# Performance work log

Hardware: AMD Instinct MI355X
Metric: run time of the kernel (lower is better)

Reference implementation:

```python
import jax, jax.numpy as jnp
import numpy as np

NP_, NG_ = 20000, 5000            # protein / go_annotation node counts
D_FEAT, D_HID, N_CLS = 512, 128, 1000
E_PP, E_PG, E_GP = 240000, 100000, 100000
NEG_SLOPE = -0.2                  # note: the repo default slope is negative
EPS = 1e-12


def _l2norm(x):
    n = jnp.linalg.norm(x, axis=1, keepdims=True)
    return x / jnp.maximum(n, EPS)


def _edge_softmax(logits, dst, n):
    # per-destination-node softmax over incoming edges, per feature channel
    m = jax.ops.segment_max(logits, dst, num_segments=n)
    e = jnp.exp(logits - m[dst])
    s = jax.ops.segment_sum(e, dst, num_segments=n)
    return e / s[dst]


def _type_attn(h_src, h_dst, src, dst, Wl, bl, Wr, br):
    # GCN-normalized aggregation onto dst nodes, then type-level attention logits,
    # broadcast back to edges (copy_u on the reversed relation graph).
    ns, nd = h_src.shape[0], h_dst.shape[0]
    ones = jnp.ones(src.shape[0], dtype=h_src.dtype)
    outdeg = jnp.clip(jax.ops.segment_sum(ones, src, num_segments=ns), 1.0)
    feat = h_src * (outdeg ** -0.5)[:, None]
    rst = jax.ops.segment_sum(feat[src], dst, num_segments=nd)
    indeg = jnp.clip(jax.ops.segment_sum(ones, dst, num_segments=nd), 1.0)
    rst = rst * (indeg ** -0.5)[:, None]
    ea = jax.nn.elu((h_dst @ Wl + bl) + (rst @ Wr + br))  # [nd, D_HID]
    return ea[dst]                                        # [E, D_HID]


def setup_inputs() -> dict:
    key = jax.random.key(0)
    ks = iter(jax.random.split(key, 40))

    def nrm(shape, s=0.05):
        return jax.random.normal(next(ks), shape, dtype=jnp.float32) * s

    def ri(n, hi):
        return jax.random.randint(next(ks), (n,), 0, hi, dtype=jnp.int32)

    zeros = lambda n: jnp.zeros((n,), jnp.float32)
    return dict(
        x_protein=jax.random.normal(next(ks), (NP_, D_FEAT), dtype=jnp.float32),
        x_go=jax.random.normal(next(ks), (NG_, N_CLS), dtype=jnp.float32),
        src_pp=ri(E_PP, NP_), dst_pp=ri(E_PP, NP_),
        src_pg=ri(E_PG, NP_), dst_pg=ri(E_PG, NG_),
        src_gp=ri(E_GP, NG_), dst_gp=ri(E_GP, NP_),
        W1p=nrm((D_FEAT, D_HID)), b1p=zeros(D_HID),
        W1g=nrm((N_CLS, D_HID)), b1g=zeros(D_HID),
        Wl_p=nrm((D_HID, D_HID)), bl_p=zeros(D_HID),
        Wl_g=nrm((D_HID, D_HID)), bl_g=zeros(D_HID),
        Wr_p=nrm((D_HID, D_HID)), br_p=zeros(D_HID),
        Wr_g=nrm((D_HID, D_HID)), br_g=zeros(D_HID),
        Wnl=nrm((D_HID, D_HID)), bnl=zeros(D_HID),
        Wnr=nrm((D_HID, D_HID)), bnr=zeros(D_HID),
        Wfc=nrm((D_HID, N_CLS)), bfc=zeros(N_CLS),
    )


def reference(x_protein, x_go, src_pp, dst_pp, src_pg, dst_pg, src_gp, dst_gp,
              W1p, b1p, W1g, b1g, Wl_p, bl_p, Wl_g, bl_g,
              Wr_p, br_p, Wr_g, br_g, Wnl, bnl, Wnr, bnr, Wfc, bfc):
    # input projection + row-wise l2 norm (dropout disabled / eval mode)
    hp = _l2norm(x_protein @ W1p + b1p)   # [NP, D_HID]
    hg = _l2norm(x_go @ W1g + b1g)        # [NG, D_HID]

    # ---- TypeAttention over each canonical etype ----
    a_pp = _type_attn(hp, hp, src_pp, dst_pp, Wl_p, bl_p, Wr_p, br_p)
    a_pg = _type_attn(hp, hg, src_pg, dst_pg, Wl_g, bl_g, Wr_p, br_p)
    a_gp = _type_attn(hg, hp, src_gp, dst_gp, Wl_p, bl_p, Wr_g, br_g)

    # homogeneous view: proteins [0,NP), go_annotation [NP,NP+NG)
    gsrc = jnp.concatenate([src_pp, src_pg, src_gp + NP_])
    gdst = jnp.concatenate([dst_pp, dst_pg + NP_, dst_gp])
    alpha = jnp.concatenate([a_pp, a_pg, a_gp], axis=0)   # [E, D_HID]
    n = NP_ + NG_
    alpha = _edge_softmax(alpha, gdst, n)

    # ---- NodeAttention on the homogeneous graph ----
    x = jnp.concatenate([hp, hg], axis=0)                 # [N, D_HID]
    hl = (x @ Wnl + bnl)[gsrc]
    hr = (x @ Wnr + bnr)[gdst]
    e = (hl + hr) * alpha
    e = jnp.where(e > 0, e, NEG_SLOPE * e)                # LeakyReLU(slope=-0.2)
    a = _edge_softmax(e, gdst, n)
    h = jax.ops.segment_sum(x[gsrc] * a, gdst, num_segments=n)

    out = h @ Wfc + bfc   # [N, N_CLS]; rows [:NP]=protein, [NP:]=go_annotation
    return out
```

## Files before the change

### kernel.cpp

```cpp
#include <hip/hip_runtime.h>
#include <math.h>

#define NP 20000
#define NG 5000
#define NTOT 25000
#define DF 512
#define NCLS 1000
#define DH 128
#define EPP 240000
#define EPG 100000
#define EGP 100000
#define ETOT 440000
#define FS 16
#define HB 16

typedef __attribute__((ext_vector_type(8))) __bf16 bf16x8;
typedef __attribute__((ext_vector_type(4))) float f32x4;

__device__ __forceinline__ void gl2lds16(const void* g, void* l) {
    __builtin_amdgcn_global_load_lds(
        (const __attribute__((address_space(1))) unsigned int*)g,
        (__attribute__((address_space(3))) unsigned int*)l, 16, 0, 0);
}

__device__ __forceinline__ float b2f(unsigned short u) {
    union { unsigned int i; float f; } c; c.i = ((unsigned int)u) << 16; return c.f;
}

__global__ __launch_bounds__(1024) void hist_part_kernel(
    const int* __restrict__ src_pp, const int* __restrict__ dst_pp,
    const int* __restrict__ src_pg, const int* __restrict__ dst_pg,
    const int* __restrict__ src_gp, const int* __restrict__ dst_gp,
    int* __restrict__ partial)
{
    __shared__ int bins[20000];
    const int job = blockIdx.y, b = blockIdx.x;
    const int* idx; int nbins, nedge; size_t pbase;
    switch (job) {
    case 0: idx = src_pp; nbins = 20000; nedge = EPP; pbase = 0;       break;
    case 1: idx = dst_pp; nbins = 20000; nedge = EPP; pbase = 320000;  break;
    case 2: idx = src_pg; nbins = 20000; nedge = EPG; pbase = 640000;  break;
    case 3: idx = dst_pg; nbins = 5000;  nedge = EPG; pbase = 960000;  break;
    case 4: idx = src_gp; nbins = 5000;  nedge = EGP; pbase = 1040000; break;
    default: idx = dst_gp; nbins = 20000; nedge = EGP; pbase = 1120000; break;
    }
    for (int i = threadIdx.x; i < nbins; i += 1024) bins[i] = 0;
    __syncthreads();
    const int chunk = (nedge + HB - 1) / HB;
    const int e0 = b * chunk, e1 = min(e0 + chunk, nedge);
    for (int e = e0 + threadIdx.x; e < e1; e += 1024) atomicAdd(&bins[idx[e]], 1);
    __syncthreads();
    int* dst = partial + pbase + (size_t)b * nbins;
    for (int i = threadIdx.x; i < nbins; i += 1024) dst[i] = bins[i];
}

__global__ __launch_bounds__(256) void hist_merge_kernel(const int* __restrict__ partial,
    int* __restrict__ outdeg_pp, int* __restrict__ indeg_pp,
    int* __restrict__ outdeg_pg, int* __restrict__ indeg_pg,
    int* __restrict__ outdeg_gp, int* __restrict__ indeg_gp,
    int* __restrict__ fill)
{
    const int job = blockIdx.y;
    const int bin = blockIdx.x * 256 + threadIdx.x;
    if (job == 6) {
        if (bin < NTOT * FS) fill[bin] = 0;
        return;
    }
    const int nbins = (job == 3 || job == 4) ? 5000 : 20000;
    if (bin >= nbins) return;
    size_t pbase; int* outp;
    switch (job) {
    case 0: pbase = 0;       outp = outdeg_pp; break;
    case 1: pbase = 320000;  outp = indeg_pp;  break;
    case 2: pbase = 640000;  outp = outdeg_pg; break;
    case 3: pbase = 960000;  outp = indeg_pg;  break;
    case 4: pbase = 1040000; outp = outdeg_gp; break;
    default: pbase = 1120000; outp = indeg_gp; break;
    }
    const int* p = partial + pbase + bin;
    int s = 0;
#pragma unroll
    for (int b = 0; b < HB; b++) s += p[(size_t)b * nbins];
    outp[bin] = s;
}

__global__ __launch_bounds__(1024) void scan_kernel(const int* __restrict__ indeg_pp,
                                                    const int* __restrict__ indeg_gp,
                                                    const int* __restrict__ indeg_pg,
                                                    int* __restrict__ row_ptr)
{
    __shared__ int part[1024];
    int t = threadIdx.x;
    const int CH = (NTOT + 1023) / 1024;
    int base = t * CH;
    auto cntf = [&](int idx) -> int {
        return (idx < NP) ? (indeg_pp[idx] + indeg_gp[idx]) : indeg_pg[idx - NP];
    };
    int s = 0;
    for (int i = 0; i < CH; i++) { int idx = base + i; if (idx < NTOT) s += cntf(idx); }
    part[t] = s;
    __syncthreads();
    for (int off = 1; off < 1024; off <<= 1) {
        int v = (t >= off) ? part[t - off] : 0;
        __syncthreads();
        part[t] += v;
        __syncthreads();
    }
    int run = (t == 0) ? 0 : part[t - 1];
    for (int i = 0; i < CH; i++) {
        int idx = base + i;
        if (idx < NTOT) { row_ptr[idx] = run; run += cntf(idx); }
    }
    if (t == 1023) row_ptr[NTOT] = part[1023];
}

__global__ void scatter_kernel(const int* __restrict__ src_pp, const int* __restrict__ dst_pp,
                               const int* __restrict__ src_pg, const int* __restrict__ dst_pg,
                               const int* __restrict__ src_gp, const int* __restrict__ dst_gp,
                               const int* __restrict__ outdeg_pp, const int* __restrict__ outdeg_pg,
                               const int* __restrict__ outdeg_gp,
                               const int* __restrict__ row_ptr, int* fill,
                               int2* __restrict__ edata)
{
    int e = blockIdx.x * blockDim.x + threadIdx.x;
    int s, d, t; float sc;
    if (e < EPP) {
        s = src_pp[e]; d = dst_pp[e]; t = 0;
        sc = rsqrtf((float)max(outdeg_pp[s], 1));
    } else if (e < EPP + EPG) {
        int i = e - EPP; s = src_pg[i]; d = NP + dst_pg[i]; t = 1;
        sc = rsqrtf((float)max(outdeg_pg[s], 1));
    } else if (e < ETOT) {
        int i = e - EPP - EPG; int sl = src_gp[i]; s = NP + sl; d = dst_gp[i]; t = 2;
        sc = rsqrtf((float)max(outdeg_gp[sl], 1));
    } else return;
    int pos = row_ptr[d] + atomicAdd(&fill[d * FS], 1);
    edata[pos] = make_int2(s | (t << 16), __float_as_int(sc));
}

__global__ __launch_bounds__(256) void conv_all_kernel(
    const float* __restrict__ xp, const float* __restrict__ xg,
    const float* W1p, const float* W1g, const float* Wlp, const float* Wrp, const float* Wrg,
    const float* Wnl, const float* Wnr, const float* Wfc,
    __bf16* __restrict__ xpb, __bf16* __restrict__ xgb,
    __bf16* w1pt, __bf16* w1gt, __bf16* wlpt, __bf16* wrpt, __bf16* wrgt,
    __bf16* wnlt, __bf16* wnrt, __bf16* wfct)
{
    const int b = blockIdx.x;
    if (b < 5008) {
        long long e = ((long long)b * 256 + threadIdx.x) * 8;
        int row = (int)(e >> 9), k = (int)(e & 511);
        __bf16 pk[8];
        if (row < NP) {
            f32x4 v0 = *(const f32x4*)(xp + (size_t)row * 512 + k);
            f32x4 v1 = *(const f32x4*)(xp + (size_t)row * 512 + k + 4);
#pragma unroll
            for (int i = 0; i < 4; i++) { pk[i] = (__bf16)v0[i]; pk[4 + i] = (__bf16)v1[i]; }
        } else {
#pragma unroll
            for (int i = 0; i < 8; i++) pk[i] = (__bf16)0.f;
        }
        *(bf16x8*)(xpb + e) = *(bf16x8*)pk;
        return;
    }
    if (b < 7536) {
        long long e = ((long long)(b - 5008) * 256 + threadIdx.x) * 8;
        int row = (int)(e >> 10), k = (int)(e & 1023);
        __bf16 pk[8];
        if (row < NG && k + 7 < 1000) {
            f32x4 v0 = *(const f32x4*)(xg + (size_t)row * 1000 + k);
            f32x4 v1 = *(const f32x4*)(xg + (size_t)row * 1000 + k + 4);
#pragma unroll
            for (int i = 0; i < 4; i++) { pk[i] = (__bf16)v0[i]; pk[4 + i] = (__bf16)v1[i]; }
        } else {
#pragma unroll
            for (int i = 0; i < 8; i++) {
                int kk = k + i;
                pk[i] = (__bf16)((row < NG && kk < 1000) ? xg[(size_t)row * 1000 + kk] : 0.f);
            }
        }
        *(bf16x8*)(xgb + e) = *(bf16x8*)pk;
        return;
    }
    int wb = b - 7536;
    int e;
    if (wb < 256)      { e = wb * 256 + threadIdx.x;          int n = e >> 9, k = e & 511;  w1pt[e] = (__bf16)W1p[(size_t)k * 128 + n]; }
    else if (wb < 768) { e = (wb - 256) * 256 + threadIdx.x;  int n = e >> 10, k = e & 1023; w1gt[e] = (__bf16)(k < 1000 ? W1g[(size_t)k * 128 + n] : 0.f); }
    else if (wb < 832) { e = (wb - 768) * 256 + threadIdx.x;  int n = e >> 7, k = e & 127;  wlpt[e] = (__bf16)Wlp[(size_t)k * 128 + n]; }
    else if (wb < 896) { e = (wb - 832) * 256 + threadIdx.x;  int n = e >> 7, k = e & 127;  wrpt[e] = (__bf16)Wrp[(size_t)k * 128 + n]; }
    else if (wb < 960) { e = (wb - 896) * 256 + threadIdx.x;  int n = e >> 7, k = e & 127;  wrgt[e] = (__bf16)Wrg[(size_t)k * 128 + n]; }
    else if (wb < 1024){ e = (wb - 960) * 256 + threadIdx.x;  int n = e >> 7, k = e & 127;  wnlt[e] = (__bf16)Wnl[(size_t)k * 128 + n]; }
    else if (wb < 1088){ e = (wb - 1024) * 256 + threadIdx.x; int n = e >> 7, k = e & 127;  wnrt[e] = (__bf16)Wnr[(size_t)k * 128 + n]; }
    else               { e = (wb - 1088) * 256 + threadIdx.x; int n = e >> 7, k = e & 127;  wfct[e] = (__bf16)(n < 1000 ? Wfc[(size_t)k * 1000 + n] : 0.f); }
}

struct GJob {
    const __bf16* A1;
    const __bf16* B1; const __bf16* B2;
    const float* b1; const float* b2;
    float* O1; __bf16* O2; __bf16* Ob;
    int M, N, Kp, ksteps;
};

template<int ACT, int DUALW, int EMIT>
__global__ __launch_bounds__(256) void gemm_bt(GJob j0, GJob j1, int split)
{
    __shared__ __align__(16) __bf16 As[64 * 32];
    __shared__ __align__(16) __bf16 Bs[128 * 32];
    __shared__ __align__(16) __bf16 B2s[DUALW ? 128 * 32 : 8];
    __shared__ float part[2][64];

    GJob j; int bx;
    if ((int)blockIdx.x < split) { j = j0; bx = blockIdx.x; }
    else { j = j1; bx = blockIdx.x - split; }

    const int tid = threadIdx.x;
    const int wave = tid >> 6, lane = tid & 63;
    const int wr = wave >> 1, wc = wave & 1;
    const int l15 = lane & 15, lh = lane >> 4;
    const int row0 = bx * 64;
    const int col0 = blockIdx.y * 128;

    const size_t aoff = (size_t)(row0 + (tid >> 2)) * j.Kp + (tid & 3) * 8;
    const size_t boff0 = (size_t)(col0 + (tid >> 2)) * j.Kp + (tid & 3) * 8;
    const size_t boff1 = boff0 + (size_t)64 * j.Kp;
    char* alds   = (char*)As + wave * 1024;
    char* blds0  = (char*)Bs + wave * 1024;
    char* blds1  = (char*)Bs + 4096 + wave * 1024;
    char* b2lds0 = (char*)B2s + wave * 1024;
    char* b2lds1 = (char*)B2s + 4096 + wave * 1024;

    f32x4 acc[2][4], acc2[2][4];
#pragma unroll
    for (int fm = 0; fm < 2; fm++)
#pragma unroll
        for (int fn = 0; fn < 4; fn++) {
            acc[fm][fn] = (f32x4)0.f;
            if (DUALW) acc2[fm][fn] = (f32x4)0.f;
        }

    for (int ks = 0; ks < j.ksteps; ks++) {
        const int k0 = ks * 32;
        __syncthreads();
        gl2lds16(j.A1 + aoff + k0, alds);
        gl2lds16(j.B1 + boff0 + k0, blds0);
        gl2lds16(j.B1 + boff1 + k0, blds1);
        if constexpr (DUALW) {
            gl2lds16(j.B2 + boff0 + k0, b2lds0);
            gl2lds16(j.B2 + boff1 + k0, b2lds1);
        }
        __syncthreads();

#pragma unroll
        for (int fm = 0; fm < 2; fm++) {
            bf16x8 a = *(const bf16x8*)&As[(wr * 32 + fm * 16 + l15) * 32 + lh * 8];
#pragma unroll
            for (int fn = 0; fn < 4; fn++) {
                bf16x8 b = *(const bf16x8*)&Bs[(wc * 64 + fn * 16 + l15) * 32 + lh * 8];
                acc[fm][fn] = __builtin_amdgcn_mfma_f32_16x16x32_bf16(a, b, acc[fm][fn], 0, 0, 0);
                if constexpr (DUALW) {
                    bf16x8 b2 = *(const bf16x8*)&B2s[(wc * 64 + fn * 16 + l15) * 32 + lh * 8];
                    acc2[fm][fn] = __builtin_amdgcn_mfma_f32_16x16x32_bf16(a, b2, acc2[fm][fn], 0, 0, 0);
                }
            }
        }
    }

    float bias[4], bias2[4];
#pragma unroll
    for (int fn = 0; fn < 4; fn++) {
        int col = col0 + wc * 64 + fn * 16 + l15;
        bias[fn] = 0.f; bias2[fn] = 0.f;
        if (col < j.N) {
            bias[fn] = j.b1[col];
            if (DUALW) bias2[fn] = j.b2[col];
        }
    }

    float vv[2][4][4];
#pragma unroll
    for (int fm = 0; fm < 2; fm++)
#pragma unroll
        for (int fn = 0; fn < 4; fn++)
#pragma unroll
            for (int r = 0; r < 4; r++) vv[fm][fn][r] = acc[fm][fn][r] + bias[fn];

    float scale[2][4];
#pragma unroll
    for (int fm = 0; fm < 2; fm++)
#pragma unroll
        for (int r = 0; r < 4; r++) scale[fm][r] = 1.f;

    if constexpr (ACT == 2) {
        float s[2][4];
#pragma unroll
        for (int fm = 0; fm < 2; fm++)
#pragma unroll
            for (int r = 0; r < 4; r++) {
                float v = 0.f;
#pragma unroll
                for (int fn = 0; fn < 4; fn++) v += vv[fm][fn][r] * vv[fm][fn][r];
                v += __shfl_xor(v, 1);
                v += __shfl_xor(v, 2);
                v += __shfl_xor(v, 4);
                v += __shfl_xor(v, 8);
                s[fm][r] = v;
            }
        __syncthreads();
        if (l15 == 0) {
#pragma unroll
            for (int fm = 0; fm < 2; fm++)
#pragma unroll
                for (int r = 0; r < 4; r++)
                    part[wc][wr * 32 + fm * 16 + lh * 4 + r] = s[fm][r];
        }
        __syncthreads();
#pragma unroll
        for (int fm = 0; fm < 2; fm++)
#pragma unroll
            for (int r = 0; r < 4; r++) {
                int rl = wr * 32 + fm * 16 + lh * 4 + r;
                float ss = part[0][rl] + part[1][rl];
                scale[fm][r] = 1.f / fmaxf(sqrtf(ss), 1e-12f);
            }
    }

#pragma unroll
    for (int fm = 0; fm < 2; fm++)
#pragma unroll
        for (int fn = 0; fn < 4; fn++)
#pragma unroll
            for (int r = 0; r < 4; r++) {
                int row = row0 + wr * 32 + fm * 16 + lh * 4 + r;
                int col = col0 + wc * 64 + fn * 16 + l15;
                if (row < j.M && col < j.N) {
                    float v = vv[fm][fn][r] * scale[fm][r];
                    if constexpr (EMIT == 0) j.O1[(size_t)row * j.N + col] = v;
                    if constexpr (EMIT == 2) j.Ob[(size_t)row * j.N + col] = (__bf16)v;
                    if constexpr (DUALW)
                        j.O2[(size_t)row * j.N + col] = (__bf16)(acc2[fm][fn][r] + bias2[fn]);
                }
            }
}

__global__ __launch_bounds__(256) void ea_wa_kernel(
    const __bf16* __restrict__ xb, const __bf16* __restrict__ rppb, const __bf16* __restrict__ rgpb,
    const __bf16* __restrict__ wl, const __bf16* __restrict__ wrp, const __bf16* __restrict__ wrg,
    const float* __restrict__ blp, const float* __restrict__ brp, const float* __restrict__ brg,
    const int* __restrict__ indeg_pp, const int* __restrict__ indeg_gp,
    float* __restrict__ wpp, float* __restrict__ wgp)
{
    __shared__ __align__(16) __bf16 A1s[64 * 32], A2s[64 * 32], A3s[64 * 32];
    __shared__ __align__(16) __bf16 B1s[128 * 32], B2s[128 * 32], B3s[128 * 32];

    const int tid = threadIdx.x;
    const int wave = tid >> 6, lane = tid & 63;
    const int wr = wave >> 1, wc = wave & 1;
    const int l15 = lane & 15, lh = lane >> 4;
    const int row0 = blockIdx.x * 64;

    const size_t aoff = (size_t)(row0 + (tid >> 2)) * 128 + (tid & 3) * 8;
    const size_t boff0 = (size_t)(tid >> 2) * 128 + (tid & 3) * 8;
    const size_t boff1 = boff0 + (size_t)64 * 128;
    char* a1 = (char*)A1s + wave * 1024;
    char* a2 = (char*)A2s + wave * 1024;
    char* a3 = (char*)A3s + wave * 1024;
    char* b1l0 = (char*)B1s + wave * 1024, *b1l1 = (char*)B1s + 4096 + wave * 1024;
    char* b2l0 = (char*)B2s + wave * 1024, *b2l1 = (char*)B2s + 4096 + wave * 1024;
    char* b3l0 = (char*)B3s + wave * 1024, *b3l1 = (char*)B3s + 4096 + wave * 1024;

    f32x4 accL[2][4], accP[2][4], accG[2][4];
#pragma unroll
    for (int fm = 0; fm < 2; fm++)
#pragma unroll
        for (int fn = 0; fn < 4; fn++) {
            accL[fm][fn] = (f32x4)0.f; accP[fm][fn] = (f32x4)0.f; accG[fm][fn] = (f32x4)0.f;
        }

    for (int ks = 0; ks < 4; ks++) {
        const int k0 = ks * 32;
        __syncthreads();
        gl2lds16(xb + aoff + k0, a1);
        gl2lds16(rppb + aoff + k0, a2);
        gl2lds16(rgpb + aoff + k0, a3);
        gl2lds16(wl + boff0 + k0, b1l0);  gl2lds16(wl + boff1 + k0, b1l1);
        gl2lds16(wrp + boff0 + k0, b2l0); gl2lds16(wrp + boff1 + k0, b2l1);
        gl2lds16(wrg + boff0 + k0, b3l0); gl2lds16(wrg + boff1 + k0, b3l1);
        __syncthreads();

#pragma unroll
        for (int fm = 0; fm < 2; fm++) {
            const int arow = (wr * 32 + fm * 16 + l15) * 32 + lh * 8;
            bf16x8 aL = *(const bf16x8*)&A1s[arow];
            bf16x8 aP = *(const bf16x8*)&A2s[arow];
            bf16x8 aG = *(const bf16x8*)&A3s[arow];
#pragma unroll
            for (int fn = 0; fn < 4; fn++) {
                const int brow = (wc * 64 + fn * 16 + l15) * 32 + lh * 8;
                bf16x8 bL = *(const bf16x8*)&B1s[brow];
                bf16x8 bP = *(const bf16x8*)&B2s[brow];
                bf16x8 bG = *(const bf16x8*)&B3s[brow];
                accL[fm][fn] = __builtin_amdgcn_mfma_f32_16x16x32_bf16(aL, bL, accL[fm][fn], 0, 0, 0);
                accP[fm][fn] = __builtin_amdgcn_mfma_f32_16x16x32_bf16(aP, bP, accP[fm][fn], 0, 0, 0);
                accG[fm][fn] = __builtin_amdgcn_mfma_f32_16x16x32_bf16(aG, bG, accG[fm][fn], 0, 0, 0);
            }
        }
    }

    float bp[4], bg[4];
#pragma unroll
    for (int fn = 0; fn < 4; fn++) {
        int col = wc * 64 + fn * 16 + l15;
        bp[fn] = blp[col] + brp[col];
        bg[fn] = blp[col] + brg[col];
    }

#pragma unroll
    for (int fm = 0; fm < 2; fm++)
#pragma unroll
        for (int r = 0; r < 4; r++) {
            int row = row0 + wr * 32 + fm * 16 + lh * 4 + r;
            int rr = min(row, NP - 1);
            int npp = indeg_pp[rr], ngp = indeg_gp[rr];
#pragma unroll
            for (int fn = 0; fn < 4; fn++) {
                int col = wc * 64 + fn * 16 + l15;
                float app = accL[fm][fn][r] + accP[fm][fn][r] + bp[fn];
                app = app > 0.f ? app : (__expf(app) - 1.f);
                float agp = accL[fm][fn][r] + accG[fm][fn][r] + bg[fn];
                agp = agp > 0.f ? agp : (__expf(agp) - 1.f);
                float wppv = 0.f, wgpv = 0.f;
                if (npp > 0 && ngp > 0) {
                    float mx = fmaxf(app, agp);
                    float ep = __expf(app - mx), eg = __expf(agp - mx);
                    float den = (float)npp * ep + (float)ngp * eg;
                    wppv = ep / den; wgpv = eg / den;
                } else if (npp > 0) wppv = 1.f / (float)npp;
                else if (ngp > 0) wgpv = 1.f / (float)ngp;
                if (row < NP) {
                    wpp[(size_t)row * DH + col] = wppv;
                    wgp[(size_t)row * DH + col] = wgpv;
                }
            }
        }
}

__global__ __launch_bounds__(128) void rst_agg_kernel(const __bf16* __restrict__ x,
                                                      const int* __restrict__ row_ptr,
                                                      const int2* __restrict__ edata,
                                                      const int* __restrict__ indeg_pp,
                                                      const int* __restrict__ indeg_gp,
                                                      __bf16* __restrict__ rppb, __bf16* __restrict__ rgpb)
{
    const int d = blockIdx.x;
    const int tid = threadIdx.x;
    const unsigned c2 = tid & 63;
    const int h = tid >> 6;
    const int beg = row_ptr[d], end = row_ptr[d + 1];
    const unsigned int* xu = (const unsigned int*)x;
    float spp0 = 0.f, spp1 = 0.f, sgp0 = 0.f, sgp1 = 0.f;

    int i = beg + h;
    for (; i + 6 < end; i += 8) {
        int2 e0 = edata[i], e1 = edata[i + 2], e2 = edata[i + 4], e3 = edata[i + 6];
        unsigned u0 = xu[(((unsigned)e0.x & 0xFFFFu) << 6) | c2];
        unsigned u1 = xu[(((unsigned)e1.x & 0xFFFFu) << 6) | c2];
        unsigned u2 = xu[(((unsigned)e2.x & 0xFFFFu) << 6) | c2];
        unsigned u3 = xu[(((unsigned)e3.x & 0xFFFFu) << 6) | c2];
#pragma unroll
        for (int k = 0; k < 4; k++) {
            unsigned u = (k == 0) ? u0 : (k == 1) ? u1 : (k == 2) ? u2 : u3;
            int2 e = (k == 0) ? e0 : (k == 1) ? e1 : (k == 2) ? e2 : e3;
            float lo = __uint_as_float(u << 16);
            float hi = __uint_as_float(u & 0xFFFF0000u);
            float sc = __int_as_float(e.y);
            if ((e.x >> 16) == 0) { spp0 = fmaf(lo, sc, spp0); spp1 = fmaf(hi, sc, spp1); }
            else                  { sgp0 = fmaf(lo, sc, sgp0); sgp1 = fmaf(hi, sc, sgp1); }
        }
    }
    for (; i < end; i += 2) {
        int2 e = edata[i];
        unsigned u = xu[(((unsigned)e.x & 0xFFFFu) << 6) | c2];
        float lo = __uint_as_float(u << 16);
        float hi = __uint_as_float(u & 0xFFFF0000u);
        float sc = __int_as_float(e.y);
        if ((e.x >> 16) == 0) { spp0 = fmaf(lo, sc, spp0); spp1 = fmaf(hi, sc, spp1); }
        else                  { sgp0 = fmaf(lo, sc, sgp0); sgp1 = fmaf(hi, sc, sgp1); }
    }

    __shared__ float red[4][64];
    if (h == 1) { red[0][c2] = spp0; red[1][c2] = spp1; red[2][c2] = sgp0; red[3][c2] = sgp1; }
    __syncthreads();
    if (h == 0) {
        spp0 += red[0][c2]; spp1 += red[1][c2]; sgp0 += red[2][c2]; sgp1 += red[3][c2];
        float ipp = rsqrtf((float)max(indeg_pp[d], 1));
        float igp = rsqrtf((float)max(indeg_gp[d], 1));
        union { unsigned u; __bf16 b[2]; } wp, wg;
        wp.b[0] = (__bf16)(spp0 * ipp); wp.b[1] = (__bf16)(spp1 * ipp);
        wg.b[0] = (__bf16)(sgp0 * igp); wg.b[1] = (__bf16)(sgp1 * igp);
        ((unsigned*)rppb)[((unsigned)d << 6) | c2] = wp.u;
        ((unsigned*)rgpb)[((unsigned)d << 6) | c2] = wg.u;
    }
}

__global__ __launch_bounds__(256) void pack_xhl_kernel(const unsigned int* __restrict__ xb2,
                                                       const unsigned int* __restrict__ hl2,
                                                       uint4* __restrict__ xhl4)
{
    int i = blockIdx.x * 256 + threadIdx.x;
    if (i >= 25024 * 128 / 4) return;
    unsigned int xa = xb2[i * 2], xbv = xb2[i * 2 + 1];
    unsigned int ha = hl2[i * 2], hbv = hl2[i * 2 + 1];
    uint4 o;
    o.x = (xa & 0xFFFFu) | (ha << 16);
    o.y = (xa >> 16) | (ha & 0xFFFF0000u);
    o.z = (xbv & 0xFFFFu) | (hbv << 16);
    o.w = (xbv >> 16) | (hbv & 0xFFFF0000u);
    xhl4[i] = o;
}

__global__ __launch_bounds__(128) void node_attn_kernel(const unsigned int* __restrict__ xhl,
                                                        const __bf16* __restrict__ hrb,
                                                        const float* __restrict__ wpp_arr,
                                                        const float* __restrict__ wgp_arr,
                                                        const int* __restrict__ indeg_pg,
                                                        const int* __restrict__ row_ptr,
                                                        const int2* __restrict__ edata,
                                                        __bf16* __restrict__ hb)
{
    const int d = blockIdx.x;
    const unsigned c = threadIdx.x;
    const int beg = row_ptr[d], end = row_ptr[d + 1];
    const float hrd = b2f(((const unsigned short*)hrb)[((size_t)d << 7) | c]);
    float wppv, wgpv;
    if (d < NP) {
        wppv = wpp_arr[((size_t)d << 7) | c];
        wgpv = wgp_arr[((size_t)d << 7) | c];
    } else {
        float w = 1.f / (float)max(indeg_pg[d - NP], 1);
        wppv = w; wgpv = w;
    }
    float ssum = 0.f, acc = 0.f;

    int i = beg;
    for (; i + 3 < end; i += 4) {
        int p0 = edata[i].x, p1 = edata[i + 1].x, p2 = edata[i + 2].x, p3 = edata[i + 3].x;
        unsigned int u0 = xhl[(((unsigned)p0 & 0xFFFFu) << 7) | c];
        unsigned int u1 = xhl[(((unsigned)p1 & 0xFFFFu) << 7) | c];
        unsigned int u2 = xhl[(((unsigned)p2 & 0xFFFFu) << 7) | c];
        unsigned int u3 = xhl[(((unsigned)p3 & 0xFFFFu) << 7) | c];
#pragma unroll
        for (int k = 0; k < 4; k++) {
            unsigned int u = (k == 0) ? u0 : (k == 1) ? u1 : (k == 2) ? u2 : u3;
            int p = (k == 0) ? p0 : (k == 1) ? p1 : (k == 2) ? p2 : p3;
            float xv  = __uint_as_float(u << 16);
            float hlv = __uint_as_float(u & 0xFFFF0000u);
            float al = ((p >> 16) == 0) ? wppv : wgpv;
            float e = (hlv + hrd) * al;
            e = fmaxf(e, -0.2f * e);
            float pw = __expf(e);
            ssum += pw;
            acc = fmaf(pw, xv, acc);
        }
    }
    for (; i < end; i++) {
        int p = edata[i].x;
        unsigned int u = xhl[(((unsigned)p & 0xFFFFu) << 7) | c];
        float xv  = __uint_as_float(u << 16);
        float hlv = __uint_as_float(u & 0xFFFF0000u);
        float al = ((p >> 16) == 0) ? wppv : wgpv;
        float e = (hlv + hrd) * al;
        e = fmaxf(e, -0.2f * e);
        float pw = __expf(e);
        ssum += pw;
        acc = fmaf(pw, xv, acc);
    }

    hb[((size_t)d << 7) | c] = (__bf16)((end > beg) ? acc / ssum : 0.f);
}

extern "C" void kernel_launch(void* const* d_in, const int* in_sizes, int n_in,
                              void* d_out, int out_size, void* d_ws, size_t ws_size,
                              hipStream_t stream)
{
    const float* x_protein = (const float*)d_in[0];
    const float* x_go      = (const float*)d_in[1];
    const int* src_pp = (const int*)d_in[2];
    const int* dst_pp = (const int*)d_in[3];
    const int* src_pg = (const int*)d_in[4];
    const int* dst_pg = (const int*)d_in[5];
    const int* src_gp = (const int*)d_in[6];
    const int* dst_gp = (const int*)d_in[7];
    const float* W1p = (const float*)d_in[8];
    const float* b1p = (const float*)d_in[9];
    const float* W1g = (const float*)d_in[10];
    const float* b1g = (const float*)d_in[11];
    const float* Wl_p = (const float*)d_in[12];
    const float* bl_p = (const float*)d_in[13];
    const float* Wr_p = (const float*)d_in[16];
    const float* br_p = (const float*)d_in[17];
    const float* Wr_g = (const float*)d_in[18];
    const float* br_g = (const float*)d_in[19];
    const float* Wnl = (const float*)d_in[20];
    const float* bnl = (const float*)d_in[21];
    const float* Wnr = (const float*)d_in[22];
    const float* bnr = (const float*)d_in[23];
    const float* Wfc = (const float*)d_in[24];
    const float* bfc = (const float*)d_in[25];
    float* out = (float*)d_out;

    size_t off = 0;
    char* base = (char*)d_ws;
    auto alloc = [&](size_t words) { void* p = base + off * 4; off += (words + 7) & ~(size_t)7; return p; };

    __bf16* xb  = (__bf16*)alloc((size_t)25024 * 128 / 2);
    __bf16* hlb = (__bf16*)alloc((size_t)25024 * 128 / 2);
    __bf16* hrb = (__bf16*)alloc((size_t)25024 * 128 / 2);
    char* U = (char*)alloc((size_t)25024 * 128);
    __bf16* rppb = (__bf16*)U;
    __bf16* rgpb = (__bf16*)(U + (size_t)20032 * 128 * 2);
    unsigned int* xhl = (unsigned int*)U;
    char* R1 = (char*)alloc((size_t)5128192 + 2588672);
    int*    partial = (int*)R1;
    __bf16* xpb = (__bf16*)R1;
    __bf16* xgb = (__bf16*)(R1 + (size_t)20032 * 512 * 2);
    float*  wpp = (float*)R1;
    float*  wgp = wpp + (size_t)20000 * 128;
    __bf16* haggb = (__bf16*)(wgp + (size_t)20000 * 128);
    __bf16* w1pt = (__bf16*)alloc(128 * 512 / 2);
    __bf16* w1gt = (__bf16*)alloc(128 * 1024 / 2);
    __bf16* wlpt = (__bf16*)alloc(128 * 128 / 2);
    __bf16* wrpt = (__bf16*)alloc(128 * 128 / 2);
    __bf16* wrgt = (__bf16*)alloc(128 * 128 / 2);
    __bf16* wnlt = (__bf16*)alloc(128 * 128 / 2);
    __bf16* wnrt = (__bf16*)alloc(128 * 128 / 2);
    __bf16* wfct = (__bf16*)alloc(1024 * 128 / 2);
    int* outdeg_pp = (int*)alloc(NP);
    int* outdeg_pg = (int*)alloc(NP);
    int* outdeg_gp = (int*)alloc(NG);
    int* indeg_pp  = (int*)alloc(NP);
    int* indeg_gp  = (int*)alloc(NP);
    int* indeg_pg  = (int*)alloc(NG);
    int* fill      = (int*)alloc((size_t)NTOT * FS);
    int* row_ptr   = (int*)alloc(NTOT + 1);
    int2* edata    = (int2*)alloc((size_t)ETOT * 2);

    hist_part_kernel<<<dim3(HB, 6), 1024, 0, stream>>>(
        src_pp, dst_pp, src_pg, dst_pg, src_gp, dst_gp, partial);
    hist_merge_kernel<<<dim3((NTOT * FS + 255) / 256, 7), 256, 0, stream>>>(
        partial, outdeg_pp, indeg_pp, outdeg_pg, indeg_pg, outdeg_gp, indeg_gp, fill);
    scan_kernel<<<1, 1024, 0, stream>>>(indeg_pp, indeg_gp, indeg_pg, row_ptr);
    scatter_kernel<<<(ETOT + 255) / 256, 256, 0, stream>>>(
        src_pp, dst_pp, src_pg, dst_pg, src_gp, dst_gp,
        outdeg_pp, outdeg_pg, outdeg_gp, row_ptr, fill, edata);
    conv_all_kernel<<<9136, 256, 0, stream>>>(
        x_protein, x_go, W1p, W1g, Wl_p, Wr_p, Wr_g, Wnl, Wnr, Wfc,
        xpb, xgb, w1pt, w1gt, wlpt, wrpt, wrgt, wnlt, wnrt, wfct);

    {
        GJob p0 = { xpb, w1pt, nullptr, b1p, nullptr, nullptr, nullptr, xb, NP, 128, 512, 16 };
        GJob p1 = { xgb, w1gt, nullptr, b1g, nullptr, nullptr, nullptr,
                    xb + (size_t)NP * 128, NG, 128, 1024, 32 };
        gemm_bt<2, 0, 2><<<392, 256, 0, stream>>>(p0, p1, 313);
    }

    rst_agg_kernel<<<NP, 128, 0, stream>>>(xb, row_ptr, edata, indeg_pp, indeg_gp, rppb, rgpb);

    {
        GJob h0 = { xb, wnlt, wnrt, bnl, bnr, nullptr, hrb, hlb, NTOT, 128, 128, 4 };
        gemm_bt<0, 1, 2><<<391, 256, 0, stream>>>(h0, h0, 1 << 30);
    }

    ea_wa_kernel<<<313, 256, 0, stream>>>(xb, rppb, rgpb, wlpt, wrpt, wrgt,
                                          bl_p, br_p, br_g, indeg_pp, indeg_gp, wpp, wgp);

    pack_xhl_kernel<<<3128, 256, 0, stream>>>((const unsigned int*)xb, (const unsigned int*)hlb, (uint4*)xhl);

    node_attn_kernel<<<NTOT, 128, 0, stream>>>(xhl, hrb, wpp, wgp, indeg_pg, row_ptr, edata, haggb);

    {
        GJob o0 = { haggb, wfct, nullptr, bfc, nullptr, out, nullptr, nullptr, NTOT, NCLS, 128, 4 };
        gemm_bt<0, 0, 0><<<dim3(391, 8), 256, 0, stream>>>(o0, o0, 1 << 30);
    }

    (void)in_sizes; (void)n_in; (void)out_size; (void)ws_size;
}
```

Before: 257.8 us.

## Fuse protein fp32→bf16 conversion into GEMM and xhl packing into epilogue

Result: faster. 247.1 us (-4.2%).

```diff
diff --git a/kernel.cpp b/kernel.cpp
--- a/kernel.cpp
+++ b/kernel.cpp
@@ -25,6 +25,11 @@
 
 __device__ __forceinline__ float b2f(unsigned short u) {
     union { unsigned int i; float f; } c; c.i = ((unsigned int)u) << 16; return c.f;
+}
+
+__device__ __forceinline__ unsigned short f2bbits(float v) {
+    __bf16 t = (__bf16)v;
+    return __builtin_bit_cast(unsigned short, t);
 }
 
 __global__ __launch_bounds__(1024) void hist_part_kernel(
@@ -139,32 +144,16 @@
 }
 
 __global__ __launch_bounds__(256) void conv_all_kernel(
-    const float* __restrict__ xp, const float* __restrict__ xg,
+    const float* __restrict__ xg,
     const float* W1p, const float* W1g, const float* Wlp, const float* Wrp, const float* Wrg,
     const float* Wnl, const float* Wnr, const float* Wfc,
-    __bf16* __restrict__ xpb, __bf16* __restrict__ xgb,
+    __bf16* __restrict__ xgb,
     __bf16* w1pt, __bf16* w1gt, __bf16* wlpt, __bf16* wrpt, __bf16* wrgt,
     __bf16* wnlt, __bf16* wnrt, __bf16* wfct)
 {
     const int b = blockIdx.x;
-    if (b < 5008) {
+    if (b < 2528) {
         long long e = ((long long)b * 256 + threadIdx.x) * 8;
-        int row = (int)(e >> 9), k = (int)(e & 511);
-        __bf16 pk[8];
-        if (row < NP) {
-            f32x4 v0 = *(const f32x4*)(xp + (size_t)row * 512 + k);
-            f32x4 v1 = *(const f32x4*)(xp + (size_t)row * 512 + k + 4);
-#pragma unroll
-            for (int i = 0; i < 4; i++) { pk[i] = (__bf16)v0[i]; pk[4 + i] = (__bf16)v1[i]; }
-        } else {
-#pragma unroll
-            for (int i = 0; i < 8; i++) pk[i] = (__bf16)0.f;
-        }
-        *(bf16x8*)(xpb + e) = *(bf16x8*)pk;
-        return;
-    }
-    if (b < 7536) {
-        long long e = ((long long)(b - 5008) * 256 + threadIdx.x) * 8;
         int row = (int)(e >> 10), k = (int)(e & 1023);
         __bf16 pk[8];
         if (row < NG && k + 7 < 1000) {
@@ -182,7 +171,7 @@
         *(bf16x8*)(xgb + e) = *(bf16x8*)pk;
         return;
     }
-    int wb = b - 7536;
+    int wb = b - 2528;
     int e;
     if (wb < 256)      { e = wb * 256 + threadIdx.x;          int n = e >> 9, k = e & 511;  w1pt[e] = (__bf16)W1p[(size_t)k * 128 + n]; }
     else if (wb < 768) { e = (wb - 256) * 256 + threadIdx.x;  int n = e >> 10, k = e & 1023; w1gt[e] = (__bf16)(k < 1000 ? W1g[(size_t)k * 128 + n] : 0.f); }
@@ -195,11 +184,11 @@
 }
 
 struct GJob {
-    const __bf16* A1;
+    const void* A1;
     const __bf16* B1; const __bf16* B2;
     const float* b1; const float* b2;
-    float* O1; __bf16* O2; __bf16* Ob;
-    int M, N, Kp, ksteps;
+    float* O1; __bf16* O2; unsigned* Oi; __bf16* Ob;
+    int M, N, Kp, ksteps, af32;
 };
 
 template<int ACT, int DUALW, int EMIT>
@@ -221,7 +210,11 @@
     const int row0 = bx * 64;
     const int col0 = blockIdx.y * 128;
 
+    const __bf16* A1b = (const __bf16*)j.A1;
+    const float*  A1f = (const float*)j.A1;
+
     const size_t aoff = (size_t)(row0 + (tid >> 2)) * j.Kp + (tid & 3) * 8;
+    const size_t afoff = (size_t)min(row0 + (tid >> 2), j.M - 1) * j.Kp + (tid & 3) * 8;
     const size_t boff0 = (size_t)(col0 + (tid >> 2)) * j.Kp + (tid & 3) * 8;
     const size_t boff1 = boff0 + (size_t)64 * j.Kp;
     char* alds   = (char*)As + wave * 1024;
@@ -242,12 +235,22 @@
     for (int ks = 0; ks < j.ksteps; ks++) {
         const int k0 = ks * 32;
         __syncthreads();
-        gl2lds16(j.A1 + aoff + k0, alds);
         gl2lds16(j.B1 + boff0 + k0, blds0);
         gl2lds16(j.B1 + boff1 + k0, blds1);
         if constexpr (DUALW) {
             gl2lds16(j.B2 + boff0 + k0, b2lds0);
             gl2lds16(j.B2 + boff1 + k0, b2lds1);
+        }
+        if (j.af32) {
+            const float* ap = A1f + afoff + k0;
+            f32x4 v0 = *(const f32x4*)ap;
+            f32x4 v1 = *(const f32x4*)(ap + 4);
+            __bf16 pk[8];
+#pragma unroll
+            for (int i = 0; i < 4; i++) { pk[i] = (__bf16)v0[i]; pk[4 + i] = (__bf16)v1[i]; }
+            *(bf16x8*)&As[(tid >> 2) * 32 + (tid & 3) * 8] = *(bf16x8*)pk;
+        } else {
+            gl2lds16(A1b + aoff + k0, alds);
         }
         __syncthreads();
 
@@ -337,6 +340,10 @@
                     float v = vv[fm][fn][r] * scale[fm][r];
                     if constexpr (EMIT == 0) j.O1[(size_t)row * j.N + col] = v;
                     if constexpr (EMIT == 2) j.Ob[(size_t)row * j.N + col] = (__bf16)v;
+                    if constexpr (EMIT == 3) {
+                        unsigned short xv = ((const unsigned short*)j.A1)[(size_t)row * 128 + col];
+                        j.Oi[(size_t)row * 128 + col] = (unsigned)xv | ((unsigned)f2bbits(v) << 16);
+                    }
                     if constexpr (DUALW)
                         j.O2[(size_t)row * j.N + col] = (__bf16)(acc2[fm][fn][r] + bias2[fn]);
                 }
@@ -501,22 +508,6 @@
         ((unsigned*)rppb)[((unsigned)d << 6) | c2] = wp.u;
         ((unsigned*)rgpb)[((unsigned)d << 6) | c2] = wg.u;
     }
-}
-
-__global__ __launch_bounds__(256) void pack_xhl_kernel(const unsigned int* __restrict__ xb2,
-                                                       const unsigned int* __restrict__ hl2,
-                                                       uint4* __restrict__ xhl4)
-{
-    int i = blockIdx.x * 256 + threadIdx.x;
-    if (i >= 25024 * 128 / 4) return;
-    unsigned int xa = xb2[i * 2], xbv = xb2[i * 2 + 1];
-    unsigned int ha = hl2[i * 2], hbv = hl2[i * 2 + 1];
-    uint4 o;
-    o.x = (xa & 0xFFFFu) | (ha << 16);
-    o.y = (xa >> 16) | (ha & 0xFFFF0000u);
-    o.z = (xbv & 0xFFFFu) | (hbv << 16);
-    o.w = (xbv >> 16) | (hbv & 0xFFFF0000u);
-    xhl4[i] = o;
 }
 
 __global__ __launch_bounds__(128) void node_attn_kernel(const unsigned int* __restrict__ xhl,
@@ -614,7 +605,6 @@
     auto alloc = [&](size_t words) { void* p = base + off * 4; off += (words + 7) & ~(size_t)7; return p; };
 
     __bf16* xb  = (__bf16*)alloc((size_t)25024 * 128 / 2);
-    __bf16* hlb = (__bf16*)alloc((size_t)25024 * 128 / 2);
     __bf16* hrb = (__bf16*)alloc((size_t)25024 * 128 / 2);
     char* U = (char*)alloc((size_t)25024 * 128);
     __bf16* rppb = (__bf16*)U;
@@ -622,8 +612,7 @@
     unsigned int* xhl = (unsigned int*)U;
     char* R1 = (char*)alloc((size_t)5128192 + 2588672);
     int*    partial = (int*)R1;
-    __bf16* xpb = (__bf16*)R1;
-    __bf16* xgb = (__bf16*)(R1 + (size_t)20032 * 512 * 2);
+    __bf16* xgb = (__bf16*)R1;
     float*  wpp = (float*)R1;
     float*  wgp = wpp + (size_t)20000 * 128;
     __bf16* haggb = (__bf16*)(wgp + (size_t)20000 * 128);
@@ -653,33 +642,34 @@
     scatter_kernel<<<(ETOT + 255) / 256, 256, 0, stream>>>(
         src_pp, dst_pp, src_pg, dst_pg, src_gp, dst_gp,
         outdeg_pp, outdeg_pg, outdeg_gp, row_ptr, fill, edata);
-    conv_all_kernel<<<9136, 256, 0, stream>>>(
-        x_protein, x_go, W1p, W1g, Wl_p, Wr_p, Wr_g, Wnl, Wnr, Wfc,
-        xpb, xgb, w1pt, w1gt, wlpt, wrpt, wrgt, wnlt, wnrt, wfct);
+    conv_all_kernel<<<4128, 256, 0, stream>>>(
+        x_go, W1p, W1g, Wl_p, Wr_p, Wr_g, Wnl, Wnr, Wfc,
+        xgb, w1pt, w1gt, wlpt, wrpt, wrgt, wnlt, wnrt, wfct);
 
     {
-        GJob p0 = { xpb, w1pt, nullptr, b1p, nullptr, nullptr, nullptr, xb, NP, 128, 512, 16 };
-        GJob p1 = { xgb, w1gt, nullptr, b1g, nullptr, nullptr, nullptr,
-                    xb + (size_t)NP * 128, NG, 128, 1024, 32 };
+        GJob p0 = { x_protein, w1pt, nullptr, b1p, nullptr, nullptr, nullptr, nullptr, xb,
+                    NP, 128, 512, 16, 1 };
+        GJob p1 = { xgb, w1gt, nullptr, b1g, nullptr, nullptr, nullptr, nullptr,
+                    xb + (size_t)NP * 128, NG, 128, 1024, 32, 0 };
         gemm_bt<2, 0, 2><<<392, 256, 0, stream>>>(p0, p1, 313);
     }
 
     rst_agg_kernel<<<NP, 128, 0, stream>>>(xb, row_ptr, edata, indeg_pp, indeg_gp, rppb, rgpb);
-
-    {
-        GJob h0 = { xb, wnlt, wnrt, bnl, bnr, nullptr, hrb, hlb, NTOT, 128, 128, 4 };
-        gemm_bt<0, 1, 2><<<391, 256, 0, stream>>>(h0, h0, 1 << 30);
-    }
 
     ea_wa_kernel<<<313, 256, 0, stream>>>(xb, rppb, rgpb, wlpt, wrpt, wrgt,
                                           bl_p, br_p, br_g, indeg_pp, indeg_gp, wpp, wgp);
 
-    pack_xhl_kernel<<<3128, 256, 0, stream>>>((const unsigned int*)xb, (const unsigned int*)hlb, (uint4*)xhl);
+    {
+        GJob h0 = { xb, wnlt, wnrt, bnl, bnr, nullptr, hrb, xhl, nullptr,
+                    NTOT, 128, 128, 4, 0 };
+        gemm_bt<0, 1, 3><<<391, 256, 0, stream>>>(h0, h0, 1 << 30);
+    }
 
     node_attn_kernel<<<NTOT, 128, 0, stream>>>(xhl, hrb, wpp, wgp, indeg_pg, row_ptr, edata, haggb);
 
     {
-        GJob o0 = { haggb, wfct, nullptr, bfc, nullptr, out, nullptr, nullptr, NTOT, NCLS, 128, 4 };
+        GJob o0 = { haggb, wfct, nullptr, bfc, nullptr, out, nullptr, nullptr, nullptr,
+                    NTOT, NCLS, 128, 4, 0 };
         gemm_bt<0, 0, 0><<<dim3(391, 8), 256, 0, stream>>>(o0, o0, 1 << 30);
     }
 
```
